# Performance work log

Measured on AMD Instinct MI355X. Metric: run time of the kernel, lower is better.

Reference implementation:

```python
import jax, jax.numpy as jnp
import numpy as np

B, O, I, D = 8, 128, 128, 1024


def setup_inputs() -> dict:
    key = jax.random.key(0)
    ks = jax.random.split(key, 10)
    s = 1.0 / np.sqrt(2 * D)  # torch Linear default-ish scale
    return {
        "output": jax.random.normal(ks[0], (B, O, D), jnp.float32),
        "context": jax.random.normal(ks[1], (B, I, D), jnp.float32),
        "mask": jax.random.randint(ks[2], (B, I), 0, 2, jnp.int32),
        # self.w = Linear(2*dim, dim), split into the output-half and context-half
        "w_out_w": jax.random.normal(ks[3], (D, D), jnp.float32) * s,
        "w_ctx_w": jax.random.normal(ks[4], (D, D), jnp.float32) * s,
        "w_b": jax.random.normal(ks[5], (D,), jnp.float32) * s,
        # self.score = Linear(dim, 1)
        "score_w": jax.random.normal(ks[6], (D,), jnp.float32) * (1.0 / np.sqrt(D)),
        "score_b": jnp.zeros((), jnp.float32),
        # self.linear_out = Linear(2*dim, dim)
        "lin_w": jax.random.normal(ks[7], (2 * D, D), jnp.float32) * s,
        "lin_b": jax.random.normal(ks[8], (D,), jnp.float32) * s,
    }


def reference(output, context, mask, w_out_w, w_ctx_w, w_b, score_w, score_b, lin_w, lin_b):
    # Additive (Bahdanau) attention.
    # cat(out, ctx) @ W^T == out @ W1 + ctx @ W2  -> avoid [B,O,I,2D] concat.
    s_out = jnp.einsum('bod,de->boe', output, w_out_w)            # [B,O,D]
    s_ctx = jnp.einsum('bid,de->bie', context, w_ctx_w)           # [B,I,D]
    h = jax.nn.leaky_relu(s_out[:, :, None, :] + s_ctx[:, None, :, :] + w_b)  # [B,O,I,D]
    score = jnp.einsum('boid,d->boi', h, score_w) + score_b       # [B,O,I]
    score = jnp.where(mask[:, None, :] == 1, -jnp.inf, score)
    attn = jax.nn.softmax(score, axis=-1)                         # [B,O,I]
    attn_output = jnp.einsum('boi,bid->bod', attn, context)       # mix=True: bmm
    # fn=True: linear_out on cat(attn_output, output) then leaky_relu
    combined = jnp.concatenate([attn_output, output], axis=-1)    # [B,O,2D]
    attn_output = jax.nn.leaky_relu(combined @ lin_w + lin_b)     # [B,O,D]
    return attn_output, attn
```

## Files before the change

### kernel.cpp

```cpp
#include <hip/hip_runtime.h>

namespace {

constexpr int kB = 8, kO = 128, kI = 128, kD = 1024;
constexpr long kOutAttnOff = (long)kB * kO * kD;

typedef __attribute__((ext_vector_type(8))) short short8;
typedef __attribute__((ext_vector_type(4))) float f32x4;
typedef __attribute__((ext_vector_type(2))) float f32x2;
typedef __attribute__((ext_vector_type(2))) unsigned u32x2;

__device__ __forceinline__ float leaky(float x) { return fmaxf(x, 0.01f * x); }

__device__ __forceinline__ short f2bf(float f) {
    unsigned u = __builtin_bit_cast(unsigned, f);
    u += 0x7FFFu + ((u >> 16) & 1u);
    return (short)(u >> 16);
}
__device__ __forceinline__ void b8tofs(const short8 v, float* f) {
    const unsigned* u = (const unsigned*)&v;
#pragma unroll
    for (int j = 0; j < 4; ++j) {
        f[2 * j]     = __builtin_bit_cast(float, u[j] << 16);
        f[2 * j + 1] = __builtin_bit_cast(float, u[j] & 0xffff0000u);
    }
}
__device__ __forceinline__ void bpair(const short8 a, const short8 b, f32x2* p) {
    float fa[8], fb[8];
    b8tofs(a, fa); b8tofs(b, fb);
#pragma unroll
    for (int j = 0; j < 8; ++j) p[j] = f32x2{fa[j], fb[j]};
}
__device__ __forceinline__ f32x2 vabs2(f32x2 x) {
    u32x2 u = __builtin_bit_cast(u32x2, x);
    u &= 0x7fffffffu;
    return __builtin_bit_cast(f32x2, u);
}

__device__ __forceinline__ void gll16(const void* g, void* l) {
    __builtin_amdgcn_global_load_lds(
        (const __attribute__((address_space(1))) int*)g,
        (__attribute__((address_space(3))) int*)l, 16, 0, 0);
}

__global__ __launch_bounds__(256)
void conv_all(const float* __restrict__ output, const float* __restrict__ context,
              const float* __restrict__ w1, const float* __restrict__ w2,
              const float* __restrict__ lin,
              short* __restrict__ ob16, short* __restrict__ cb16,
              short* __restrict__ w1t, short* __restrict__ w2t,
              short* __restrict__ lint)
{
    __shared__ float T[64][68];
    const int bid = blockIdx.x, tid = threadIdx.x;

    if (bid < 1024) {
        const int idx = bid * 256 + tid;
        const float* src; short* dst; int i;
        if (idx < (1 << 17)) { src = output;  dst = ob16; i = idx; }
        else                 { src = context; dst = cb16; i = idx - (1 << 17); }
        const float4* s4 = (const float4*)src + (long)i * 2;
        const float4 v0 = s4[0], v1 = s4[1];
        short8 r;
        r[0] = f2bf(v0.x); r[1] = f2bf(v0.y); r[2] = f2bf(v0.z); r[3] = f2bf(v0.w);
        r[4] = f2bf(v1.x); r[5] = f2bf(v1.y); r[6] = f2bf(v1.z); r[7] = f2bf(v1.w);
        *(short8*)(dst + (long)i * 8) = r;
        return;
    }

    const int tb = bid - 1024;
    const float* src; short* dst; long C, R; int t2;
    if (tb < 256)      { src = w1;  dst = w1t;  R = 1024; C = 1024; t2 = tb; }
    else if (tb < 512) { src = w2;  dst = w2t;  R = 1024; C = 1024; t2 = tb - 256; }
    else               { src = lin; dst = lint; R = 2048; C = 1024; t2 = tb - 512; }
    const int tr = t2 >> 4, tc = t2 & 15;
    const int r = tid >> 2, q = tid & 3;

    const float* s = src + (long)(tr * 64 + r) * C + tc * 64 + q * 16;
    const float4 a0 = ((const float4*)s)[0];
    const float4 a1 = ((const float4*)s)[1];
    const float4 a2 = ((const float4*)s)[2];
    const float4 a3 = ((const float4*)s)[3];
    *(float4*)&T[r][q * 16 + 0]  = a0;
    *(float4*)&T[r][q * 16 + 4]  = a1;
    *(float4*)&T[r][q * 16 + 8]  = a2;
    *(float4*)&T[r][q * 16 + 12] = a3;
    __syncthreads();

    short8 o0, o1;
#pragma unroll
    for (int j = 0; j < 8; ++j)  o0[j] = f2bf(T[q * 16 + j][r]);
#pragma unroll
    for (int j = 0; j < 8; ++j)  o1[j] = f2bf(T[q * 16 + 8 + j][r]);
    short* dp = dst + (long)(tc * 64 + r) * R + tr * 64 + q * 16;
    *(short8*)dp       = o0;
    *((short8*)dp + 1) = o1;
}

__global__ __launch_bounds__(256, 4)
void mm_jobs(const short* __restrict__ ob16, const short* __restrict__ cb16,
             const short* __restrict__ w1t, const short* __restrict__ w2t,
             const short* __restrict__ lint,
             const float* __restrict__ w_b, const float* __restrict__ lin_b,
             float* __restrict__ s_out, short* __restrict__ s_ctx16,
             float* __restrict__ outlin, short* __restrict__ ctxlin)
{
    __shared__ short As[2][64][64];
    __shared__ short Bs[2][64][64];
    const int tid = threadIdx.x;
    const int t = (blockIdx.x & 7) * 128 + (blockIdx.x >> 3);
    const int lane = tid & 63, w = tid >> 6;

    const short *Ap, *Bp;
    int lda, ldb, bm, bn, ldc;
    const float* bias = nullptr;
    float* Cf = nullptr;
    short* Ch = nullptr;

    if (t < 768) {
        const int job = t >> 8, tl = t & 255;
        bm = (tl & 15) * 64;
        bn = (tl >> 4) * 64;
        lda = 1024; ldb = 1024; ldc = 1024;
        if (job == 0)      { Ap = ob16; Bp = w1t;         bias = w_b;   Cf = s_out;   }
        else if (job == 1) { Ap = ob16; Bp = lint + 1024; ldb = 2048; bias = lin_b; Cf = outlin; }
        else               { Ap = cb16; Bp = w2t;                       Ch = s_ctx16; }
    } else {
        const int tl = t - 768, bz = tl >> 5, t2 = tl & 31;
        bm = (t2 & 15) * 64;
        bn = (t2 >> 4) * 64;
        Ap = lint; lda = 2048;
        Bp = cb16 + (long)bz * (kI * kD); ldb = 1024;
        Ch = ctxlin + (long)bz * (kD * kI); ldc = 128;
    }

    const int m0 = (w >> 1) * 32, n0 = (w & 1) * 32;
    const int fr = lane & 15, fcol = lane >> 4, sl = lane & 7;
    const int r8 = lane >> 3;
    const int sw8 = ((lane & 7) ^ r8) * 8;
    const int w16 = w * 16;

    f32x4 acc[2][2] = {};

    auto stage = [&](int buf, int k0) {
        const short* ga = Ap + (long)(bm + w16 + r8) * lda + k0 + sw8;
        gll16(ga,                 &As[buf][w16][0]);
        gll16(ga + 8 * (long)lda, &As[buf][w16 + 8][0]);
        const short* gb = Bp + (long)(bn + w16 + r8) * ldb + k0 + sw8;
        gll16(gb,                 &Bs[buf][w16][0]);
        gll16(gb + 8 * (long)ldb, &Bs[buf][w16 + 8][0]);
    };

    stage(0, 0);
    __syncthreads();
    int cur = 0;
    for (int s = 0; s < 16; ++s) {
        if (s < 15) stage(cur ^ 1, (s + 1) << 6);
#pragma unroll
        for (int ks8 = 0; ks8 < 8; ks8 += 4) {
            const int sa = ((ks8 + fcol) ^ sl) * 8;
            short8 a[2], b[2];
#pragma unroll
            for (int mi = 0; mi < 2; ++mi)
                a[mi] = *(const short8*)&As[cur][m0 + mi * 16 + fr][sa];
#pragma unroll
            for (int ni = 0; ni < 2; ++ni)
                b[ni] = *(const short8*)&Bs[cur][n0 + ni * 16 + fr][sa];
#pragma unroll
            for (int mi = 0; mi < 2; ++mi)
#pragma unroll
                for (int ni = 0; ni < 2; ++ni)
                    acc[mi][ni] = __builtin_amdgcn_mfma_f32_16x16x32_bf16(
                        a[mi], b[ni], acc[mi][ni], 0, 0, 0);
        }
        __syncthreads();
        cur ^= 1;
    }

    float bv[2] = {0, 0};
    if (bias) {
#pragma unroll
        for (int ni = 0; ni < 2; ++ni) bv[ni] = bias[bn + n0 + ni * 16 + fr];
    }
#pragma unroll
    for (int mi = 0; mi < 2; ++mi)
#pragma unroll
        for (int ni = 0; ni < 2; ++ni)
#pragma unroll
            for (int r = 0; r < 4; ++r) {
                const int row = bm + m0 + mi * 16 + ((lane >> 4) << 2) + r;
                const int col = bn + n0 + ni * 16 + fr;
                const float v = acc[mi][ni][r] + bv[ni];
                if (Ch) Ch[(long)row * ldc + col] = f2bf(v);
                else    Cf[(long)row * ldc + col] = v;
            }
}

__global__ __launch_bounds__(256, 3)
void score_final(const float* __restrict__ s_out, const short* __restrict__ s_ctx16,
                 const float* __restrict__ score_w, const float* __restrict__ score_b,
                 const int* __restrict__ mask, const short* __restrict__ ctxlin,
                 const float* __restrict__ outlin, float* __restrict__ out_main,
                 float* __restrict__ attn_f32)
{
    __shared__ float As[2][1032];
    __shared__ __align__(16) char CsPool[32768];
    __shared__ short Wsh[1032];
    __shared__ float Ps[4][2][128];
    __shared__ float Psi[4][128];
    __shared__ float so_sh[2];
    __shared__ int   Msk[128];
    __shared__ __align__(16) short Pl[16][136];

    short* CsS = (short*)CsPool;
    const int b   = blockIdx.x;
    const int o0  = blockIdx.y * 2;
    const int tid = threadIdx.x;
    const int wv  = tid >> 6;
    const int ln  = tid & 63;
    const int fr  = ln & 15, fg = ln >> 4;

    const short* crow = s_ctx16 + (long)b * kI * kD;
    auto stageCs = [&](int slot, int dc) {
#pragma unroll
        for (int it = 0; it < 4; ++it) {
            const int rb = wv * 32 + it * 8;
            const int r  = rb + (ln >> 3);
            const int sc = (ln & 7) ^ (r & 7);
            gll16(crow + (long)r * kD + dc + sc * 8, CsS + slot * 8192 + rb * 64);
        }
    };

    stageCs(0, 0);

    const float* arow = s_out + (long)(b * kO + o0) * kD;
#pragma unroll
    for (int q = 0; q < 2; ++q) {
        const int tq = tid + q * 256;
        const int rr = tq >> 8, c4 = (tq & 255) * 4;
        *(float4*)&As[rr][c4] = *(const float4*)&arow[(long)rr * kD + c4];
    }
    {
        const float4 w4 = *(const float4*)&score_w[tid * 4];
        const unsigned p0 = (unsigned)(unsigned short)f2bf(w4.x)
                          | ((unsigned)(unsigned short)f2bf(w4.y) << 16);
        const unsigned p1 = (unsigned)(unsigned short)f2bf(w4.z)
                          | ((unsigned)(unsigned short)f2bf(w4.w) << 16);
        *(u32x2*)&Wsh[tid * 4] = u32x2{p0, p1};
    }
    if (tid < 128) Msk[tid] = mask[b * kI + tid];
    {
        short* pf = &Pl[0][0];
        for (int j = tid; j < 272; j += 256) *(short8*)(pf + j * 8) = short8{};
    }
    __syncthreads();

    if (wv < 2) {
        const short8 wA = *(const short8*)&Wsh[ln * 16];
        const short8 wB = *(const short8*)&Wsh[ln * 16 + 8];
        float wf[16];
        b8tofs(wA, wf); b8tofs(wB, wf + 8);
        float acc = 0.0f;
#pragma unroll
        for (int q = 0; q < 4; ++q) {
            const float4 av = *(const float4*)&As[wv][ln * 16 + q * 4];
            acc = fmaf(av.x, wf[q*4+0], acc); acc = fmaf(av.y, wf[q*4+1], acc);
            acc = fmaf(av.z, wf[q*4+2], acc); acc = fmaf(av.w, wf[q*4+3], acc);
        }
#pragma unroll
        for (int d = 1; d < 64; d <<= 1) acc += __shfl_xor(acc, d, 64);
        if (ln == 0) so_sh[wv] = acc;
    }

    f32x2 si2{0.0f, 0.0f};
    f32x2 sa2[2] = {f32x2{0.0f, 0.0f}, f32x2{0.0f, 0.0f}};
    const int kb = wv * 16;

    int buf = 0;
    for (int c = 0; c < 16; ++c) {
        const int dc = c * 64;
        if (c < 15) stageCs(buf ^ 1, dc + 64);
        const short* Cb = CsS + buf * 8192;
        const int sc0 = ((wv * 2 + 0) ^ (ln & 7)) * 8;
        const int sc1 = ((wv * 2 + 1) ^ (ln & 7)) * 8;
        const short8 cA0 = *(const short8*)&Cb[ln * 64 + sc0];
        const short8 cA1 = *(const short8*)&Cb[ln * 64 + sc1];
        const short8 cB0 = *(const short8*)&Cb[(ln + 64) * 64 + sc0];
        const short8 cB1 = *(const short8*)&Cb[(ln + 64) * 64 + sc1];
        f32x2 c2[16];
        bpair(cA0, cB0, c2);
        bpair(cA1, cB1, c2 + 8);
        const short8 w0 = *(const short8*)&Wsh[dc + kb];
        const short8 w1 = *(const short8*)&Wsh[dc + kb + 8];
        float wr[16];
        b8tofs(w0, wr); b8tofs(w1, wr + 8);
        float av0[16], av1[16];
#pragma unroll
        for (int q = 0; q < 4; ++q) {
            *(float4*)&av0[q * 4] = *(const float4*)&As[0][dc + kb + q * 4];
            *(float4*)&av1[q * 4] = *(const float4*)&As[1][dc + kb + q * 4];
        }
#pragma unroll
        for (int d = 0; d < 16; ++d) {
            const f32x2 w2 = {wr[d], wr[d]};
            si2 += c2[d] * w2;
            const f32x2 x0 = c2[d] + f32x2{av0[d], av0[d]};
            const f32x2 x1 = c2[d] + f32x2{av1[d], av1[d]};
            sa2[0] += vabs2(x0) * w2;
            sa2[1] += vabs2(x1) * w2;
        }
        __syncthreads();
        buf ^= 1;
    }

    short* Bsh = (short*)CsPool;
    const short* ctxb = ctxlin + (long)b * (kD * kI);
    auto stageB = [&](int half, int nc) {
#pragma unroll
        for (int it = 0; it < 4; ++it) {
            const int rb = wv * 16 + it * 4;
            const int r  = rb + (ln >> 4);
            const int n  = nc * 64 + r;
            const int sc = (ln & 15) ^ (r & 7);
            gll16(ctxb + (long)n * kI + sc * 8, Bsh + half * 8192 + rb * kI);
        }
    };
    stageB(0, 0);

#pragma unroll
    for (int o = 0; o < 2; ++o) {
        Ps[wv][o][ln]      = sa2[o].x;
        Ps[wv][o][ln + 64] = sa2[o].y;
    }
    Psi[wv][ln]      = si2.x;
    Psi[wv][ln + 64] = si2.y;
    __syncthreads();

    if (wv < 2) {
        const int ow = wv;
        const float negInf = -__builtin_huge_valf();
        const float sb = score_b[0];
        const float siT0 = Psi[0][ln] + Psi[1][ln] + Psi[2][ln] + Psi[3][ln];
        const float siT1 = Psi[0][ln + 64] + Psi[1][ln + 64]
                         + Psi[2][ln + 64] + Psi[3][ln + 64];
        const float saT0 = Ps[0][ow][ln] + Ps[1][ow][ln]
                         + Ps[2][ow][ln] + Ps[3][ow][ln];
        const float saT1 = Ps[0][ow][ln + 64] + Ps[1][ow][ln + 64]
                         + Ps[2][ow][ln + 64] + Ps[3][ow][ln + 64];
        const float soV = so_sh[ow];
        float s0 = 0.505f * (soV + siT0) + 0.495f * saT0 + sb;
        float s1 = 0.505f * (soV + siT1) + 0.495f * saT1 + sb;
        if (Msk[ln]      != 0) s0 = negInf;
        if (Msk[ln + 64] != 0) s1 = negInf;

        float m = fmaxf(s0, s1);
#pragma unroll
        for (int d = 1; d < 64; d <<= 1) m = fmaxf(m, __shfl_xor(m, d, 64));
        const float e0 = __expf(s0 - m);
        const float e1 = __expf(s1 - m);
        float sum = e0 + e1;
#pragma unroll
        for (int d = 1; d < 64; d <<= 1) sum += __shfl_xor(sum, d, 64);
        const float inv = 1.0f / sum;

        const long rowoff = (long)(b * kO + o0 + ow) * kI;
        const float p0 = e0 * inv, p1 = e1 * inv;
        attn_f32[rowoff + ln]      = p0;
        attn_f32[rowoff + ln + 64] = p1;
        Pl[ow][ln]      = f2bf(p0);
        Pl[ow][ln + 64] = f2bf(p1);
    }
    __syncthreads();

    for (int nc = 0; nc < 16; ++nc) {
        if (nc < 15) {
            stageB((nc + 1) & 1, nc + 1);
            asm volatile("s_waitcnt vmcnt(4)" ::: "memory");
        } else {
            asm volatile("s_waitcnt vmcnt(0)" ::: "memory");
        }
        __builtin_amdgcn_sched_barrier(0);
        const short* Bc = Bsh + (nc & 1) * 8192;
        f32x4 acc{};
#pragma unroll
        for (int ks = 0; ks < 4; ++ks) {
            const short8 a = *(const short8*)&Pl[fr][ks * 32 + fg * 8];
            const int sc = ((ks * 4 + fg) ^ (fr & 7)) * 8;
            const short8 bb = *(const short8*)&Bc[(wv * 16 + fr) * kI + sc];
            acc = __builtin_amdgcn_mfma_f32_16x16x32_bf16(a, bb, acc, 0, 0, 0);
        }
        if (fg == 0) {
#pragma unroll
            for (int r = 0; r < 2; ++r) {
                const int n = nc * 64 + wv * 16 + fr;
                const long off = (long)(b * kO + o0 + r) * kD + n;
                out_main[off] = leaky(acc[r] + outlin[off]);
            }
        }
    }
}

}

extern "C" void kernel_launch(void* const* d_in, const int* in_sizes, int n_in,
                              void* d_out, int out_size, void* d_ws, size_t ws_size,
                              hipStream_t stream)
{
    const float* output  = (const float*)d_in[0];
    const float* context = (const float*)d_in[1];
    const int*   mask    = (const int*)d_in[2];
    const float* w_out_w = (const float*)d_in[3];
    const float* w_ctx_w = (const float*)d_in[4];
    const float* w_b     = (const float*)d_in[5];
    const float* score_w = (const float*)d_in[6];
    const float* score_b = (const float*)d_in[7];
    const float* lin_w   = (const float*)d_in[8];
    const float* lin_b   = (const float*)d_in[9];

    float* out_main = (float*)d_out;
    float* out_attn = out_main + kOutAttnOff;
    float* s_out    = out_main;

    char* wp = (char*)d_ws;
    short* s_ctx16 = (short*)wp;  wp += (size_t)2 << 20;
    short* ob16    = (short*)wp;  wp += (size_t)2 << 20;
    short* cb16    = (short*)wp;  wp += (size_t)2 << 20;
    short* w1t     = (short*)wp;  wp += (size_t)2 << 20;
    short* w2t     = (short*)wp;  wp += (size_t)2 << 20;
    short* lint    = (short*)wp;  wp += (size_t)4 << 20;
    float* outlin  = (float*)wp;  wp += (size_t)4 << 20;
    short* ctxlin  = (short*)wp;

    const dim3 blk(256);

    hipLaunchKernelGGL(conv_all, dim3(2048), blk, 0, stream,
        output, context, w_out_w, w_ctx_w, lin_w, ob16, cb16, w1t, w2t, lint);

    hipLaunchKernelGGL(mm_jobs, dim3(1024), blk, 0, stream,
        ob16, cb16, w1t, w2t, lint, w_b, lin_b, s_out, s_ctx16, outlin, ctxlin);

    hipLaunchKernelGGL(score_final, dim3(8, 64), blk, 0, stream,
        s_out, s_ctx16, score_w, score_b, mask, ctxlin, outlin, out_main, out_attn);
}
```

Measured before the change: 59.64 us.

## Give each wave private LDS staging slices to drop block-wide barriers

The context-staging loop now has each wave load only the 16-column slice it consumes into its own LDS region. It waits with vmcnt instead of __syncthreads, which removes the per-chunk block barrier. The B-staging for the final bmm likewise uses per-wave LDS slices. The trade-off is narrower 16-byte-pair global reads per row, and correctness now relies on the asynchronous LDS loads being visible to the wave once vmcnt completes.

```diff
diff --git a/kernel.cpp b/kernel.cpp
--- a/kernel.cpp
+++ b/kernel.cpp
@@ -219,15 +219,18 @@
     const int wv  = tid >> 6;
     const int ln  = tid & 63;
     const int fr  = ln & 15, fg = ln >> 4;
+    const int kb  = wv * 16;
+    short* CsW = CsS + wv * 4096;
 
     const short* crow = s_ctx16 + (long)b * kI * kD;
-    auto stageCs = [&](int slot, int dc) {
+    auto stageCs = [&](int slot, int c) {
+        const int dc = c * 64;
+        short* dst = CsW + slot * 2048;
 #pragma unroll
         for (int it = 0; it < 4; ++it) {
-            const int rb = wv * 32 + it * 8;
-            const int r  = rb + (ln >> 3);
-            const int sc = (ln & 7) ^ (r & 7);
-            gll16(crow + (long)r * kD + dc + sc * 8, CsS + slot * 8192 + rb * 64);
+            const int row  = it * 32 + (ln >> 1);
+            const int half = ln & 1;
+            gll16(crow + (long)row * kD + dc + kb + half * 8, dst + it * 512);
         }
     };
 
@@ -274,19 +277,21 @@
 
     f32x2 si2{0.0f, 0.0f};
     f32x2 sa2[2] = {f32x2{0.0f, 0.0f}, f32x2{0.0f, 0.0f}};
-    const int kb = wv * 16;
-
-    int buf = 0;
+
     for (int c = 0; c < 16; ++c) {
+        if (c < 15) {
+            stageCs((c + 1) & 1, c + 1);
+            asm volatile("s_waitcnt vmcnt(4)" ::: "memory");
+        } else {
+            asm volatile("s_waitcnt vmcnt(0)" ::: "memory");
+        }
+        __builtin_amdgcn_sched_barrier(0);
         const int dc = c * 64;
-        if (c < 15) stageCs(buf ^ 1, dc + 64);
-        const short* Cb = CsS + buf * 8192;
-        const int sc0 = ((wv * 2 + 0) ^ (ln & 7)) * 8;
-        const int sc1 = ((wv * 2 + 1) ^ (ln & 7)) * 8;
-        const short8 cA0 = *(const short8*)&Cb[ln * 64 + sc0];
-        const short8 cA1 = *(const short8*)&Cb[ln * 64 + sc1];
-        const short8 cB0 = *(const short8*)&Cb[(ln + 64) * 64 + sc0];
-        const short8 cB1 = *(const short8*)&Cb[(ln + 64) * 64 + sc1];
+        const short* Cw = CsW + (c & 1) * 2048;
+        const short8 cA0 = *(const short8*)&Cw[ln * 16];
+        const short8 cA1 = *(const short8*)&Cw[ln * 16 + 8];
+        const short8 cB0 = *(const short8*)&Cw[(ln + 64) * 16];
+        const short8 cB1 = *(const short8*)&Cw[(ln + 64) * 16 + 8];
         f32x2 c2[16];
         bpair(cA0, cB0, c2);
         bpair(cA1, cB1, c2 + 8);
@@ -309,20 +314,17 @@
             sa2[0] += vabs2(x0) * w2;
             sa2[1] += vabs2(x1) * w2;
         }
-        __syncthreads();
-        buf ^= 1;
-    }
-
-    short* Bsh = (short*)CsPool;
+    }
+
     const short* ctxb = ctxlin + (long)b * (kD * kI);
-    auto stageB = [&](int half, int nc) {
+    auto stageB = [&](int slot, int nc) {
+        short* dst = CsW + slot * 2048;
 #pragma unroll
         for (int it = 0; it < 4; ++it) {
-            const int rb = wv * 16 + it * 4;
-            const int r  = rb + (ln >> 4);
-            const int n  = nc * 64 + r;
-            const int sc = (ln & 15) ^ (r & 7);
-            gll16(ctxb + (long)n * kI + sc * 8, Bsh + half * 8192 + rb * kI);
+            const int rl = it * 4 + (ln >> 4);
+            const int n  = nc * 64 + wv * 16 + rl;
+            gll16(ctxb + (long)n * kI + ((ln & 15) ^ (rl & 7)) * 8,
+                  dst + it * 512);
         }
     };
     stageB(0, 0);
@@ -380,13 +382,13 @@
             asm volatile("s_waitcnt vmcnt(0)" ::: "memory");
         }
         __builtin_amdgcn_sched_barrier(0);
-        const short* Bc = Bsh + (nc & 1) * 8192;
+        const short* Bc = CsW + (nc & 1) * 2048;
         f32x4 acc{};
 #pragma unroll
         for (int ks = 0; ks < 4; ++ks) {
             const short8 a = *(const short8*)&Pl[fr][ks * 32 + fg * 8];
             const int sc = ((ks * 4 + fg) ^ (fr & 7)) * 8;
-            const short8 bb = *(const short8*)&Bc[(wv * 16 + fr) * kI + sc];
+            const short8 bb = *(const short8*)&Bc[fr * 128 + sc];
             acc = __builtin_amdgcn_mfma_f32_16x16x32_bf16(a, bb, acc, 0, 0, 0);
         }
         if (fg == 0) {
```

New measurement: 58.11 us. -2.6%, faster.
